# Kernel tuning notes

Hardware: AMD Instinct MI355X
Metric: run time of the kernel (lower is better)

The kernel has to match this reference:

```python
import jax, jax.numpy as jnp
import numpy as np

B, N, C, NS = 4, 2048, 128, 64
RADIUS = 0.25
BN_EPS = 1e-5


def _ball_query(xyz):
    """First-NS point indices within RADIUS of each point (pointnet2 semantics:
    indices taken in ascending point order, short balls padded with the first hit).
    xyz: (B,N,3) -> idx: (B,N,NS) int32."""
    sq = jnp.sum(xyz * xyz, axis=-1)                                   # (B,N)
    d2 = sq[:, :, None] + sq[:, None, :] - 2.0 * jnp.einsum('bnd,bmd->bnm', xyz, xyz)
    within = d2 < RADIUS ** 2                                          # (B,N,N)
    cand = jnp.where(within, jnp.arange(N, dtype=jnp.int32)[None, None, :], N)
    idx = jnp.sort(cand, axis=-1)[..., :NS]                            # first NS hits
    idx = jnp.where(idx == N, idx[..., :1], idx)                       # pad with first hit
    return idx


def _bn_relu(h, g, b):
    # eval-mode BatchNorm2d with running_mean=0, running_var=1, then ReLU
    inv = 1.0 / jnp.sqrt(1.0 + BN_EPS)
    return jax.nn.relu(g[None, :, None, None] * (h * inv) + b[None, :, None, None])


def _forward(xyz, features, W1, W2, W3, g1, g2, g3, b1, b2, b3):
    idx = _ball_query(xyz)                                             # (B,N,NS)
    bidx = jnp.arange(B)[:, None, None]
    g_xyz = xyz[bidx, idx]                                             # (B,N,NS,3)
    grouped_xyz = jnp.transpose(g_xyz - xyz[:, :, None, :], (0, 3, 1, 2))  # (B,3,N,NS) relative
    feat_t = jnp.transpose(features, (0, 2, 1))                        # (B,N,C)
    g_feat = jnp.transpose(feat_t[bidx, idx], (0, 3, 1, 2))            # (B,C,N,NS)
    grouped_features = jnp.concatenate([grouped_xyz, g_feat], axis=1)  # (B,3+C,N,NS)

    xyz_feature = jnp.concatenate([jnp.transpose(xyz, (0, 2, 1)), features], axis=1)  # (B,3+C,N)
    center = jax.lax.stop_gradient(xyz_feature)[..., None]             # .detach() in torch
    diff = grouped_features - center
    h = diff * diff                                                    # squared diff

    h = _bn_relu(jnp.einsum('oc,bcns->bons', W1, h), g1, b1)           # (B,256,N,NS)
    h = _bn_relu(jnp.einsum('oc,bcns->bons', W2, h), g2, b2)           # (B,128,N,NS)
    h = _bn_relu(jnp.einsum('oc,bcns->bons', W3, h), g3, b3)           # (B,1,N,NS)

    shift = jnp.sum(grouped_xyz * h, axis=-1)                          # (B,3,N)
    return shift / jnp.sum(h, axis=-1)                                 # / (B,1,N)


def setup_inputs() -> dict:
    key = jax.random.key(0)
    ks = jax.random.split(key, 5)
    cin = C + 3
    return {
        'xyz': jax.random.uniform(ks[0], (B, N, 3), dtype=jnp.float32),
        'features': jax.random.normal(ks[1], (B, C, N), dtype=jnp.float32),
        'W1': jax.random.normal(ks[2], (256, cin), dtype=jnp.float32) * np.float32(np.sqrt(2.0 / cin)),
        'W2': jax.random.normal(ks[3], (128, 256), dtype=jnp.float32) * np.float32(np.sqrt(2.0 / 256)),
        'W3': jax.random.normal(ks[4], (1, 128), dtype=jnp.float32) * np.float32(np.sqrt(2.0 / 128)),
        'g1': jnp.ones((256,), jnp.float32), 'g2': jnp.ones((128,), jnp.float32), 'g3': jnp.ones((1,), jnp.float32),
        'b1': jnp.zeros((256,), jnp.float32), 'b2': jnp.zeros((128,), jnp.float32), 'b3': jnp.zeros((1,), jnp.float32),
    }


def reference(xyz, features, W1, W2, W3, g1, g2, g3, b1, b2, b3):
    return _forward(xyz, features, W1, W2, W3, g1, g2, g3, b1, b2, b3)
```

## Files before the change

kernel.cpp:

```cpp
#include <hip/hip_runtime.h>
#include <math.h>

typedef _Float16 f16;
typedef _Float16 f16x8 __attribute__((ext_vector_type(8)));
typedef _Float16 f16x4 __attribute__((ext_vector_type(4)));
typedef float f32x4 __attribute__((ext_vector_type(4)));

#define B_  4
#define N_  2048
#define C_  128
#define NS_ 64

#define WS_FEAT16 0u
#define WS_IDX    2097152u
#define WS_W1X    3145728u
#define WS_W1P    3153920u
#define WS_W2P    3219456u

#define OFF_H   0
#define OFF_HX  16384
#define OFF_W   18432
#define OFF_A2  0
#define OFF_GX  51200
#define OFF_QF  51968
#define OFF_IDX 52480
#define OFF_RED 52480
#define OFF_W3  52736
#define LDS_TOTAL 53248

__device__ __forceinline__ void gl_lds16(const char* gp, char* lp) {
  __builtin_amdgcn_global_load_lds(
      (const __attribute__((address_space(1))) unsigned int*)gp,
      (__attribute__((address_space(3))) unsigned int*)lp, 16, 0, 0);
}

__device__ __forceinline__ unsigned pk2(float a, float b) {
  union { f16 h[2]; unsigned u; } cv;
  cv.h[0] = (f16)a; cv.h[1] = (f16)b;
  return cv.u;
}

__global__ __launch_bounds__(256) void prep_kernel(
    const float* __restrict__ feat, const float* __restrict__ W1,
    const float* __restrict__ W2, f16* __restrict__ feat16,
    char* __restrict__ W1x, char* __restrict__ W1p, char* __restrict__ W2p)
{
  int i = blockIdx.x * 256 + threadIdx.x;
  {
    int n = i & (N_ - 1);
    int bc = i >> 11;
    int c = bc & (C_ - 1);
    int b = bc >> 7;
    feat16[(size_t)((b << 11) + n) * C_ + c] = (f16)feat[i];
  }
  if (i < 16384) {
    int g = i >> 12, r = i & 4095, o = r >> 4, j = r & 15;
    const float* row = W1 + o * 131 + 3 + g * 32 + 2 * j;
    unsigned byte = ((unsigned)(o * 64 + j * 4)) ^ ((unsigned)(((o >> 1) & 7) << 4));
    *(unsigned*)(W1p + (size_t)g * 16384 + byte) = pk2(row[0], row[1]);
  }
  if (i < 16384) {
    int ko = i >> 12, r = i & 4095, p = r >> 5, j = r & 31;
    int o = ko * 64 + 2 * j;
    unsigned byte = ((unsigned)(p * 128 + j * 4)) ^ ((unsigned)(((p >> 1) & 7) << 4));
    *(unsigned*)(W2p + (size_t)ko * 16384 + byte) = pk2(W2[p * 256 + o], W2[p * 256 + o + 1]);
  }
  if (i < 2048) {
    int o = i >> 3, j = i & 7;
    unsigned v = 0;
    if (j == 0)      v = pk2(W1[o * 131 + 0], W1[o * 131 + 1]);
    else if (j == 1) v = pk2(W1[o * 131 + 2], 0.0f);
    *(unsigned*)(W1x + o * 32 + j * 4) = v;
  }
}

__global__ __launch_bounds__(256) void ballquery_kernel(
    const float* __restrict__ xyz, unsigned short* __restrict__ idxout)
{
  __shared__ float  xl[N_ * 3];
  __shared__ double sq[N_];
  __shared__ int    ibuf[4][NS_];

  const int b  = blockIdx.x >> 9;
  const int ng = blockIdx.x & 511;
  const int t  = threadIdx.x;
  const float* xb = xyz + (size_t)b * N_ * 3;

  for (int i = t; i < N_ * 3; i += 256) xl[i] = xb[i];
  __syncthreads();
  for (int i = t; i < N_; i += 256) {
    double x = (double)xl[3*i], y = (double)xl[3*i+1], z = (double)xl[3*i+2];
    sq[i] = x*x + y*y + z*z;
  }
  __syncthreads();

  const int wv = t >> 6, lane = t & 63;
  const int n = ng * 4 + wv;
  const double xn = (double)xl[3*n], yn = (double)xl[3*n+1], zn = (double)xl[3*n+2];
  const double sn = sq[n];

  int cnt = 0;
  for (int mb = 0; mb < N_; mb += 64) {
    int m = mb + lane;
    double dot = xn*(double)xl[3*m] + yn*(double)xl[3*m+1] + zn*(double)xl[3*m+2];
    double d2 = (sn + sq[m]) - 2.0 * dot;
    bool hit = d2 < 0.0625;
    unsigned long long mask = __ballot(hit);
    int pos = __popcll(mask & ((1ULL << lane) - 1ULL));
    int slot = cnt + pos;
    if (hit && slot < NS_) ibuf[wv][slot] = m;
    cnt += (int)__popcll(mask);
    if (cnt >= NS_) break;
  }
  asm volatile("s_waitcnt lgkmcnt(0)" ::: "memory");
  int total = cnt < NS_ ? cnt : NS_;
  int v = ibuf[wv][lane < total ? lane : 0];
  idxout[((size_t)b * N_ + n) * NS_ + lane] = (unsigned short)v;
}

__global__ __launch_bounds__(256, 3) void mlp_kernel(
    const float* __restrict__ xyz, const f16* __restrict__ feat16,
    const char* __restrict__ w1x, const char* __restrict__ w1p,
    const char* __restrict__ w2p,
    const unsigned short* __restrict__ idxg,
    const float* __restrict__ W3g,
    const float* __restrict__ g1, const float* __restrict__ b1,
    const float* __restrict__ g2, const float* __restrict__ b2,
    const float* __restrict__ g3, const float* __restrict__ b3,
    float* __restrict__ out)
{
  __shared__ __attribute__((aligned(128))) char lds[LDS_TOTAL];

  const int bidRaw = blockIdx.x;
  const int bn = ((bidRaw & 7) << 10) + (bidRaw >> 3);
  const int b = bn >> 11;
  const int n = bn & (N_ - 1);
  const int t = threadIdx.x;
  const int w = t >> 6, lane = t & 63;
  const int l15 = lane & 15, lg = lane >> 4;
  const unsigned swzl = (unsigned)(((l15 >> 1) & 7) << 4);
  const unsigned labase = ((unsigned)(l15 * 64 + lg * 16)) ^ swzl;
  const unsigned w2b0 = ((unsigned)(l15 * 128 + lg * 16)) ^ swzl;
  const unsigned w2b1 = ((unsigned)(l15 * 128 + 64 + lg * 16)) ^ swzl;
  const float inv = 1.0f / sqrtf(1.0f + 1e-5f);

  float gg1v[4], bo1v[4];
  #pragma unroll
  for (int nt = 0; nt < 4; ++nt) {
    int o = (nt >> 1) * 128 + 32 * w + (nt & 1) * 16 + l15;
    gg1v[nt] = g1[o] * inv; bo1v[nt] = b1[o];
  }
  float gg2v[2], bo2v[2];
  #pragma unroll
  for (int nt = 0; nt < 2; ++nt) {
    int p = 32 * w + nt * 16 + l15;
    gg2v[nt] = g2[p] * inv; bo2v[nt] = b2[p];
  }
  const float g3c = g3[0] * inv, b3c = b3[0];
  const float xn0 = xyz[(size_t)bn*3+0], xn1 = xyz[(size_t)bn*3+1], xn2 = xyz[(size_t)bn*3+2];

  auto STAGE = [&](int sl) {
    const char* gp; int nloads;
    if (sl == 0)      { gp = w1x;                          nloads = 2; }
    else if (sl <= 4) { gp = w1p + (size_t)(sl - 1) * 16384; nloads = 4; }
    else              { gp = w2p + (size_t)(sl - 5) * 16384; nloads = 4; }
    gp += t * 16;
    char* lp = lds + OFF_W + ((sl & 1) << 14) + (w << 10);
    for (int i = 0; i < nloads; ++i)
      gl_lds16(gp + i * 4096, lp + i * 4096);
  };

  f32x4 acc1[4][4];
  f32x4 acc2[4][2] = {};

  STAGE(0);
  if (t < 64) ((int*)(lds + OFF_IDX))[t] = (int)idxg[(size_t)bn * 64 + t];
  if (t < 64) ((unsigned*)(lds + OFF_QF))[t] =
      ((const unsigned*)(feat16 + (size_t)bn * C_))[t];
  if (t < 128) ((float*)(lds + OFF_W3))[t] = W3g[t];
  __syncthreads();

  const int* idxl = (const int*)(lds + OFF_IDX);

  {
    int s = t & 63, g = t >> 6;
    int m = idxl[s];
    const f16* pb = feat16 + ((size_t)b * N_ + m) * C_ + g * 32;
    const f16* qb = (const f16*)(lds + OFF_QF) + g * 32;
    const unsigned sw = ((unsigned)((s >> 1) & 7)) << 4;
    const unsigned base = (unsigned)(g * 4096);
    #pragma unroll
    for (int qq = 0; qq < 4; ++qq) {
      f16x8 p = *(const f16x8*)(pb + qq * 8);
      f16x8 q = *(const f16x8*)(qb + qq * 8);
      f16x8 d = p - q;
      f16x8 hh = d * d;
      unsigned byte = base
        + ((((unsigned)(s * 64 + qq * 16)) ^ sw ^ ((unsigned)((g & 3) << 4))));
      *(f16x8*)(lds + OFF_H + byte) = hh;
    }
  }
  if (t < 64) {
    int s = t;
    int m = idxl[s];
    const float* pm = xyz + ((size_t)b * N_ + m) * 3;
    float p0 = pm[0], p1 = pm[1], p2c = pm[2];
    float* gxp = (float*)(lds + OFF_GX) + s * 3;
    gxp[0] = p0 - xn0; gxp[1] = p1 - xn1; gxp[2] = p2c - xn2;
    float h0 = p0 - 2.0f * xn0; h0 *= h0;
    float h1 = p1 - 2.0f * xn1; h1 *= h1;
    float h2 = p2c - 2.0f * xn2; h2 *= h2;
    char* hx = lds + OFF_HX + s * 32;
    *(unsigned*)(hx + 0)  = pk2(h0, h1);
    *(unsigned*)(hx + 4)  = pk2(h2, 0.0f);
    *(unsigned*)(hx + 8)  = 0u;
    *(unsigned*)(hx + 12) = 0u;
    f32x4 z4 = {0.0f, 0.0f, 0.0f, 0.0f};
    *(f32x4*)(hx + 16) = z4;
  }

  STAGE(1);
  asm volatile("s_waitcnt vmcnt(4) lgkmcnt(0)" ::: "memory");
  __builtin_amdgcn_s_barrier();
  {
    const char* wbx = lds + OFF_W;
    f16x4 bf4[4];
    #pragma unroll
    for (int nt = 0; nt < 4; ++nt) {
      int orow = (nt >> 1) * 128 + 32 * w + (nt & 1) * 16 + l15;
      bf4[nt] = *(const f16x4*)(wbx + orow * 32 + lg * 8);
    }
    asm volatile("s_waitcnt lgkmcnt(0)" ::: "memory");
    __builtin_amdgcn_s_barrier();
    f16x4 af4[4];
    #pragma unroll
    for (int mt = 0; mt < 4; ++mt)
      af4[mt] = *(const f16x4*)(lds + OFF_HX + (16 * mt + l15) * 32 + lg * 8);
    const f32x4 z4 = {0.0f, 0.0f, 0.0f, 0.0f};
    #pragma unroll
    for (int mt = 0; mt < 4; ++mt)
      #pragma unroll
      for (int nt = 0; nt < 4; ++nt)
        acc1[mt][nt] = __builtin_amdgcn_mfma_f32_16x16x16f16(af4[mt], bf4[nt], z4, 0, 0, 0);
  }

  #pragma unroll
  for (int g = 0; g < 4; ++g) {
    const int sl = 1 + g;
    STAGE(sl + 1);
    asm volatile("s_waitcnt vmcnt(4) lgkmcnt(0)" ::: "memory");
    __builtin_amdgcn_s_barrier();
    const char* wb = lds + OFF_W + ((sl & 1) << 14);
    f16x8 bf[4];
    #pragma unroll
    for (int nt = 0; nt < 4; ++nt) {
      int ob = (nt >> 1) * 128 + 32 * w + (nt & 1) * 16;
      bf[nt] = *(const f16x8*)(wb + ob * 64 + labase);
    }
    asm volatile("s_waitcnt lgkmcnt(0)" ::: "memory");
    __builtin_amdgcn_s_barrier();
    const char* hb = lds + OFF_H + g * 4096;
    const unsigned gx4 = ((unsigned)g) << 4;
    f16x8 af[4];
    #pragma unroll
    for (int mt = 0; mt < 4; ++mt)
      af[mt] = *(const f16x8*)(hb + mt * 1024 + (labase ^ gx4));
    __builtin_amdgcn_s_setprio(1);
    #pragma unroll
    for (int mt = 0; mt < 4; ++mt)
      #pragma unroll
      for (int nt = 0; nt < 4; ++nt)
        acc1[mt][nt] = __builtin_amdgcn_mfma_f32_16x16x32_f16(af[mt], bf[nt], acc1[mt][nt], 0, 0, 0);
    __builtin_amdgcn_s_setprio(0);
  }

  auto EPI1 = [&](int hf) {
    #pragma unroll
    for (int mt = 0; mt < 4; ++mt)
      #pragma unroll
      for (int nt2 = 0; nt2 < 2; ++nt2) {
        const int nt = hf * 2 + nt2;
        #pragma unroll
        for (int r = 0; r < 4; ++r) {
          int s = mt * 16 + lg * 4 + r;
          float a = fmaf(acc1[mt][nt][r], gg1v[nt], bo1v[nt]);
          a = a > 0.0f ? a : 0.0f;
          unsigned byte = (unsigned)(w * 4096)
            + (((unsigned)(s * 64 + nt2 * 32 + l15 * 2)) ^ ((unsigned)(((s >> 1) & 7) << 4))
               ^ ((unsigned)((w & 3) << 4)));
          *(f16*)(lds + OFF_H + byte) = (f16)a;
        }
      }
  };
  asm volatile("s_waitcnt lgkmcnt(0)" ::: "memory");
  __builtin_amdgcn_s_barrier();
  EPI1(0);
  asm volatile("s_waitcnt lgkmcnt(0)" ::: "memory");
  __builtin_amdgcn_s_barrier();

  #pragma unroll
  for (int k = 0; k < 4; ++k) {
    const int sl = 5 + k;
    if (sl < 8) {
      STAGE(sl + 1);
      asm volatile("s_waitcnt vmcnt(4) lgkmcnt(0)" ::: "memory");
    } else {
      asm volatile("s_waitcnt vmcnt(0) lgkmcnt(0)" ::: "memory");
    }
    __builtin_amdgcn_s_barrier();
    const char* wb = lds + OFF_W + ((sl & 1) << 14);
    f16x8 bq0[2], bq1[2];
    #pragma unroll
    for (int nt2 = 0; nt2 < 2; ++nt2) {
      int pb = (32 * w + nt2 * 16) * 128;
      bq0[nt2] = *(const f16x8*)(wb + pb + w2b0);
      bq1[nt2] = *(const f16x8*)(wb + pb + w2b1);
    }
    asm volatile("s_waitcnt lgkmcnt(0)" ::: "memory");
    __builtin_amdgcn_s_barrier();
    const int sl0 = (2 * k) & 3, sl1 = (2 * k + 1) & 3;
    f16x8 a0f[4], a1f[4];
    #pragma unroll
    for (int mt = 0; mt < 4; ++mt) {
      a0f[mt] = *(const f16x8*)(lds + OFF_H + sl0 * 4096 + mt * 1024 + (labase ^ (unsigned)(sl0 << 4)));
      a1f[mt] = *(const f16x8*)(lds + OFF_H + sl1 * 4096 + mt * 1024 + (labase ^ (unsigned)(sl1 << 4)));
    }
    __builtin_amdgcn_s_setprio(1);
    #pragma unroll
    for (int mt = 0; mt < 4; ++mt)
      #pragma unroll
      for (int nt2 = 0; nt2 < 2; ++nt2) {
        f32x4 c = acc2[mt][nt2];
        c = __builtin_amdgcn_mfma_f32_16x16x32_f16(a0f[mt], bq0[nt2], c, 0, 0, 0);
        c = __builtin_amdgcn_mfma_f32_16x16x32_f16(a1f[mt], bq1[nt2], c, 0, 0, 0);
        acc2[mt][nt2] = c;
      }
    __builtin_amdgcn_s_setprio(0);
    if (k == 1) {
      asm volatile("s_waitcnt lgkmcnt(0)" ::: "memory");
      __builtin_amdgcn_s_barrier();
      EPI1(1);
      asm volatile("s_waitcnt lgkmcnt(0)" ::: "memory");
      __builtin_amdgcn_s_barrier();
    }
  }
  asm volatile("s_waitcnt lgkmcnt(0)" ::: "memory");
  __builtin_amdgcn_s_barrier();

  #pragma unroll
  for (int mt = 0; mt < 4; ++mt)
    #pragma unroll
    for (int nt2 = 0; nt2 < 2; ++nt2) {
      int p2 = 32 * w + nt2 * 16 + l15;
      #pragma unroll
      for (int r = 0; r < 4; ++r) {
        int s = mt * 16 + lg * 4 + r;
        float a = fmaf(acc2[mt][nt2][r], gg2v[nt2], bo2v[nt2]);
        a = a > 0.0f ? a : 0.0f;
        *(float*)(lds + OFF_A2 + s * 528 + p2 * 4) = a;
      }
    }
  asm volatile("s_waitcnt lgkmcnt(0)" ::: "memory");
  __builtin_amdgcn_s_barrier();

  {
    int s3 = t >> 2, q3 = t & 3;
    const float* a2row = (const float*)(lds + OFF_A2) + s3 * 132;
    const float* w3r = (const float*)(lds + OFF_W3);
    float z3 = 0.0f;
    #pragma unroll
    for (int i = 0; i < 8; ++i) {
      f32x4 av = *(const f32x4*)(a2row + q3 * 32 + i * 4);
      f32x4 wv = *(const f32x4*)(w3r + q3 * 32 + i * 4);
      z3 = fmaf(av[0], wv[0], z3); z3 = fmaf(av[1], wv[1], z3);
      z3 = fmaf(av[2], wv[2], z3); z3 = fmaf(av[3], wv[3], z3);
    }
    z3 += __shfl_xor(z3, 1);
    z3 += __shfl_xor(z3, 2);
    float wgt = fmaf(g3c, z3, b3c);
    wgt = wgt > 0.0f ? wgt : 0.0f;
    float v0 = 0.f, v1 = 0.f, v2 = 0.f, v3 = 0.f;
    if (q3 == 0) {
      const float* gx = (const float*)(lds + OFF_GX) + s3 * 3;
      v0 = gx[0] * wgt; v1 = gx[1] * wgt; v2 = gx[2] * wgt; v3 = wgt;
    }
    #pragma unroll
    for (int off = 4; off < 64; off <<= 1) {
      v0 += __shfl_xor(v0, off); v1 += __shfl_xor(v1, off);
      v2 += __shfl_xor(v2, off); v3 += __shfl_xor(v3, off);
    }
    if (lane == 0) {
      float* red = (float*)(lds + OFF_RED);
      red[w * 4 + 0] = v0; red[w * 4 + 1] = v1;
      red[w * 4 + 2] = v2; red[w * 4 + 3] = v3;
    }
    __syncthreads();
    if (t == 0) {
      const float* red = (const float*)(lds + OFF_RED);
      float n0 = red[0] + red[4] + red[8]  + red[12];
      float n1 = red[1] + red[5] + red[9]  + red[13];
      float n2 = red[2] + red[6] + red[10] + red[14];
      float dd = red[3] + red[7] + red[11] + red[15];
      out[(size_t)(b * 3 + 0) * N_ + n] = n0 / dd;
      out[(size_t)(b * 3 + 1) * N_ + n] = n1 / dd;
      out[(size_t)(b * 3 + 2) * N_ + n] = n2 / dd;
    }
  }
}

extern "C" void kernel_launch(void* const* d_in, const int* in_sizes, int n_in,
                              void* d_out, int out_size, void* d_ws, size_t ws_size,
                              hipStream_t stream) {
  (void)in_sizes; (void)n_in; (void)out_size; (void)ws_size;
  const float* xyz      = (const float*)d_in[0];
  const float* features = (const float*)d_in[1];
  const float* W1 = (const float*)d_in[2];
  const float* W2 = (const float*)d_in[3];
  const float* W3 = (const float*)d_in[4];
  const float* g1 = (const float*)d_in[5];
  const float* g2 = (const float*)d_in[6];
  const float* g3 = (const float*)d_in[7];
  const float* b1 = (const float*)d_in[8];
  const float* b2 = (const float*)d_in[9];
  const float* b3 = (const float*)d_in[10];
  float* out = (float*)d_out;

  char* ws = (char*)d_ws;
  f16* feat16         = (f16*)(ws + WS_FEAT16);
  unsigned short* idx = (unsigned short*)(ws + WS_IDX);
  char* W1x           = ws + WS_W1X;
  char* W1p           = ws + WS_W1P;
  char* W2p           = ws + WS_W2P;

  prep_kernel<<<dim3((B_ * C_ * N_) / 256), dim3(256), 0, stream>>>(
      features, W1, W2, feat16, W1x, W1p, W2p);
  ballquery_kernel<<<dim3(B_ * N_ / 4), dim3(256), 0, stream>>>(xyz, idx);
  mlp_kernel<<<dim3(B_ * N_), dim3(256), 0, stream>>>(
      xyz, feat16, W1x, W1p, W2p, idx, W3, g1, b1, g2, b2, g3, b3, out);
}
```

Before: 136.2 us.

## Fold BN scales into weights, seed accumulators with bias, trim barriers

Multiplies the BatchNorm gamma scale into W1, W2 and W3 during weight prep and starts the MFMA accumulators at the bias, so the epilogues reduce to a plain ReLU. It also changes the W2 LDS swizzle pattern to avoid bank conflicts and rearranges the barrier and prefetch order. Each stage now waits for all loads (vmcnt(0)) behind a single barrier before issuing the next prefetch, which removes one barrier per stage. The trade-off is that prefetch overlap shrinks, since the next stage's loads are only issued after the wait.

```diff
diff --git a/kernel.cpp b/kernel.cpp
--- a/kernel.cpp
+++ b/kernel.cpp
@@ -42,9 +42,12 @@
 
 __global__ __launch_bounds__(256) void prep_kernel(
     const float* __restrict__ feat, const float* __restrict__ W1,
-    const float* __restrict__ W2, f16* __restrict__ feat16,
+    const float* __restrict__ W2,
+    const float* __restrict__ g1, const float* __restrict__ g2,
+    f16* __restrict__ feat16,
     char* __restrict__ W1x, char* __restrict__ W1p, char* __restrict__ W2p)
 {
+  const float inv = 1.0f / sqrtf(1.0f + 1e-5f);
   int i = blockIdx.x * 256 + threadIdx.x;
   {
     int n = i & (N_ - 1);
@@ -55,21 +58,25 @@
   }
   if (i < 16384) {
     int g = i >> 12, r = i & 4095, o = r >> 4, j = r & 15;
+    float sc = g1[o] * inv;
     const float* row = W1 + o * 131 + 3 + g * 32 + 2 * j;
     unsigned byte = ((unsigned)(o * 64 + j * 4)) ^ ((unsigned)(((o >> 1) & 7) << 4));
-    *(unsigned*)(W1p + (size_t)g * 16384 + byte) = pk2(row[0], row[1]);
+    *(unsigned*)(W1p + (size_t)g * 16384 + byte) = pk2(row[0] * sc, row[1] * sc);
   }
   if (i < 16384) {
     int ko = i >> 12, r = i & 4095, p = r >> 5, j = r & 31;
+    float sc = g2[p] * inv;
     int o = ko * 64 + 2 * j;
-    unsigned byte = ((unsigned)(p * 128 + j * 4)) ^ ((unsigned)(((p >> 1) & 7) << 4));
-    *(unsigned*)(W2p + (size_t)ko * 16384 + byte) = pk2(W2[p * 256 + o], W2[p * 256 + o + 1]);
+    unsigned byte = ((unsigned)(p * 128 + j * 4)) ^ ((unsigned)((p & 7) << 4));
+    *(unsigned*)(W2p + (size_t)ko * 16384 + byte) =
+        pk2(W2[p * 256 + o] * sc, W2[p * 256 + o + 1] * sc);
   }
   if (i < 2048) {
     int o = i >> 3, j = i & 7;
+    float sc = g1[o] * inv;
     unsigned v = 0;
-    if (j == 0)      v = pk2(W1[o * 131 + 0], W1[o * 131 + 1]);
-    else if (j == 1) v = pk2(W1[o * 131 + 2], 0.0f);
+    if (j == 0)      v = pk2(W1[o * 131 + 0] * sc, W1[o * 131 + 1] * sc);
+    else if (j == 1) v = pk2(W1[o * 131 + 2] * sc, 0.0f);
     *(unsigned*)(W1x + o * 32 + j * 4) = v;
   }
 }
@@ -124,8 +131,8 @@
     const char* __restrict__ w2p,
     const unsigned short* __restrict__ idxg,
     const float* __restrict__ W3g,
-    const float* __restrict__ g1, const float* __restrict__ b1,
-    const float* __restrict__ g2, const float* __restrict__ b2,
+    const float* __restrict__ b1,
+    const float* __restrict__ b2,
     const float* __restrict__ g3, const float* __restrict__ b3,
     float* __restrict__ out)
 {
@@ -140,21 +147,22 @@
   const int l15 = lane & 15, lg = lane >> 4;
   const unsigned swzl = (unsigned)(((l15 >> 1) & 7) << 4);
   const unsigned labase = ((unsigned)(l15 * 64 + lg * 16)) ^ swzl;
-  const unsigned w2b0 = ((unsigned)(l15 * 128 + lg * 16)) ^ swzl;
-  const unsigned w2b1 = ((unsigned)(l15 * 128 + 64 + lg * 16)) ^ swzl;
+  const unsigned swz2 = (unsigned)((l15 & 7) << 4);
+  const unsigned w2b0 = ((unsigned)(l15 * 128 + lg * 16)) ^ swz2;
+  const unsigned w2b1 = ((unsigned)(l15 * 128 + 64 + lg * 16)) ^ swz2;
   const float inv = 1.0f / sqrtf(1.0f + 1e-5f);
 
-  float gg1v[4], bo1v[4];
+  float bo1v[4];
   #pragma unroll
   for (int nt = 0; nt < 4; ++nt) {
     int o = (nt >> 1) * 128 + 32 * w + (nt & 1) * 16 + l15;
-    gg1v[nt] = g1[o] * inv; bo1v[nt] = b1[o];
-  }
-  float gg2v[2], bo2v[2];
+    bo1v[nt] = b1[o];
+  }
+  float bo2v[2];
   #pragma unroll
   for (int nt = 0; nt < 2; ++nt) {
     int p = 32 * w + nt * 16 + l15;
-    gg2v[nt] = g2[p] * inv; bo2v[nt] = b2[p];
+    bo2v[nt] = b2[p];
   }
   const float g3c = g3[0] * inv, b3c = b3[0];
   const float xn0 = xyz[(size_t)bn*3+0], xn1 = xyz[(size_t)bn*3+1], xn2 = xyz[(size_t)bn*3+2];
@@ -171,13 +179,20 @@
   };
 
   f32x4 acc1[4][4];
-  f32x4 acc2[4][2] = {};
+  f32x4 acc2[4][2];
+  #pragma unroll
+  for (int mt = 0; mt < 4; ++mt)
+    #pragma unroll
+    for (int nt2 = 0; nt2 < 2; ++nt2) {
+      f32x4 c = {bo2v[nt2], bo2v[nt2], bo2v[nt2], bo2v[nt2]};
+      acc2[mt][nt2] = c;
+    }
 
   STAGE(0);
   if (t < 64) ((int*)(lds + OFF_IDX))[t] = (int)idxg[(size_t)bn * 64 + t];
   if (t < 64) ((unsigned*)(lds + OFF_QF))[t] =
       ((const unsigned*)(feat16 + (size_t)bn * C_))[t];
-  if (t < 128) ((float*)(lds + OFF_W3))[t] = W3g[t];
+  if (t < 128) ((float*)(lds + OFF_W3))[t] = W3g[t] * g3c;
   __syncthreads();
 
   const int* idxl = (const int*)(lds + OFF_IDX);
@@ -219,9 +234,9 @@
     *(f32x4*)(hx + 16) = z4;
   }
 
+  asm volatile("s_waitcnt vmcnt(0) lgkmcnt(0)" ::: "memory");
+  __builtin_amdgcn_s_barrier();
   STAGE(1);
-  asm volatile("s_waitcnt vmcnt(4) lgkmcnt(0)" ::: "memory");
-  __builtin_amdgcn_s_barrier();
   {
     const char* wbx = lds + OFF_W;
     f16x4 bf4[4];
@@ -230,26 +245,25 @@
       int orow = (nt >> 1) * 128 + 32 * w + (nt & 1) * 16 + l15;
       bf4[nt] = *(const f16x4*)(wbx + orow * 32 + lg * 8);
     }
-    asm volatile("s_waitcnt lgkmcnt(0)" ::: "memory");
-    __builtin_amdgcn_s_barrier();
     f16x4 af4[4];
     #pragma unroll
     for (int mt = 0; mt < 4; ++mt)
       af4[mt] = *(const f16x4*)(lds + OFF_HX + (16 * mt + l15) * 32 + lg * 8);
-    const f32x4 z4 = {0.0f, 0.0f, 0.0f, 0.0f};
     #pragma unroll
     for (int mt = 0; mt < 4; ++mt)
       #pragma unroll
-      for (int nt = 0; nt < 4; ++nt)
-        acc1[mt][nt] = __builtin_amdgcn_mfma_f32_16x16x16f16(af4[mt], bf4[nt], z4, 0, 0, 0);
+      for (int nt = 0; nt < 4; ++nt) {
+        f32x4 cb = {bo1v[nt], bo1v[nt], bo1v[nt], bo1v[nt]};
+        acc1[mt][nt] = __builtin_amdgcn_mfma_f32_16x16x16f16(af4[mt], bf4[nt], cb, 0, 0, 0);
+      }
   }
 
   #pragma unroll
   for (int g = 0; g < 4; ++g) {
     const int sl = 1 + g;
+    asm volatile("s_waitcnt vmcnt(0) lgkmcnt(0)" ::: "memory");
+    __builtin_amdgcn_s_barrier();
     STAGE(sl + 1);
-    asm volatile("s_waitcnt vmcnt(4) lgkmcnt(0)" ::: "memory");
-    __builtin_amdgcn_s_barrier();
     const char* wb = lds + OFF_W + ((sl & 1) << 14);
     f16x8 bf[4];
     #pragma unroll
@@ -257,8 +271,6 @@
       int ob = (nt >> 1) * 128 + 32 * w + (nt & 1) * 16;
       bf[nt] = *(const f16x8*)(wb + ob * 64 + labase);
     }
-    asm volatile("s_waitcnt lgkmcnt(0)" ::: "memory");
-    __builtin_amdgcn_s_barrier();
     const char* hb = lds + OFF_H + g * 4096;
     const unsigned gx4 = ((unsigned)g) << 4;
     f16x8 af[4];
@@ -283,7 +295,7 @@
         #pragma unroll
         for (int r = 0; r < 4; ++r) {
           int s = mt * 16 + lg * 4 + r;
-          float a = fmaf(acc1[mt][nt][r], gg1v[nt], bo1v[nt]);
+          float a = acc1[mt][nt][r];
           a = a > 0.0f ? a : 0.0f;
           unsigned byte = (unsigned)(w * 4096)
             + (((unsigned)(s * 64 + nt2 * 32 + l15 * 2)) ^ ((unsigned)(((s >> 1) & 7) << 4))
@@ -295,19 +307,13 @@
   asm volatile("s_waitcnt lgkmcnt(0)" ::: "memory");
   __builtin_amdgcn_s_barrier();
   EPI1(0);
-  asm volatile("s_waitcnt lgkmcnt(0)" ::: "memory");
-  __builtin_amdgcn_s_barrier();
 
   #pragma unroll
   for (int k = 0; k < 4; ++k) {
     const int sl = 5 + k;
-    if (sl < 8) {
-      STAGE(sl + 1);
-      asm volatile("s_waitcnt vmcnt(4) lgkmcnt(0)" ::: "memory");
-    } else {
-      asm volatile("s_waitcnt vmcnt(0) lgkmcnt(0)" ::: "memory");
-    }
+    asm volatile("s_waitcnt vmcnt(0) lgkmcnt(0)" ::: "memory");
     __builtin_amdgcn_s_barrier();
+    if (sl < 8) STAGE(sl + 1);
     const char* wb = lds + OFF_W + ((sl & 1) << 14);
     f16x8 bq0[2], bq1[2];
     #pragma unroll
@@ -316,8 +322,6 @@
       bq0[nt2] = *(const f16x8*)(wb + pb + w2b0);
       bq1[nt2] = *(const f16x8*)(wb + pb + w2b1);
     }
-    asm volatile("s_waitcnt lgkmcnt(0)" ::: "memory");
-    __builtin_amdgcn_s_barrier();
     const int sl0 = (2 * k) & 3, sl1 = (2 * k + 1) & 3;
     f16x8 a0f[4], a1f[4];
     #pragma unroll
@@ -340,8 +344,6 @@
       asm volatile("s_waitcnt lgkmcnt(0)" ::: "memory");
       __builtin_amdgcn_s_barrier();
       EPI1(1);
-      asm volatile("s_waitcnt lgkmcnt(0)" ::: "memory");
-      __builtin_amdgcn_s_barrier();
     }
   }
   asm volatile("s_waitcnt lgkmcnt(0)" ::: "memory");
@@ -355,7 +357,7 @@
       #pragma unroll
       for (int r = 0; r < 4; ++r) {
         int s = mt * 16 + lg * 4 + r;
-        float a = fmaf(acc2[mt][nt2][r], gg2v[nt2], bo2v[nt2]);
+        float a = acc2[mt][nt2][r];
         a = a > 0.0f ? a : 0.0f;
         *(float*)(lds + OFF_A2 + s * 528 + p2 * 4) = a;
       }
@@ -377,7 +379,7 @@
     }
     z3 += __shfl_xor(z3, 1);
     z3 += __shfl_xor(z3, 2);
-    float wgt = fmaf(g3c, z3, b3c);
+    float wgt = z3 + b3c;
     wgt = wgt > 0.0f ? wgt : 0.0f;
     float v0 = 0.f, v1 = 0.f, v2 = 0.f, v3 = 0.f;
     if (q3 == 0) {
@@ -433,8 +435,8 @@
   char* W2p           = ws + WS_W2P;
 
   prep_kernel<<<dim3((B_ * C_ * N_) / 256), dim3(256), 0, stream>>>(
-      features, W1, W2, feat16, W1x, W1p, W2p);
+      features, W1, W2, g1, g2, feat16, W1x, W1p, W2p);
   ballquery_kernel<<<dim3(B_ * N_ / 4), dim3(256), 0, stream>>>(xyz, idx);
   mlp_kernel<<<dim3(B_ * N_), dim3(256), 0, stream>>>(
-      xyz, feat16, W1x, W1p, W2p, idx, W3, g1, b1, g2, b2, g3, b3, out);
-}
+      xyz, feat16, W1x, W1p, W2p, idx, W3, b1, b2, g3, b3, out);
+}
```

New measurement: 136.3 us. About the same (+0.1%).
